# Performance work log

Measured on AMD Instinct MI355X. Metric: run time of the kernel, lower is better.

## Reference

```python
import jax, jax.numpy as jnp
import numpy as np

EPS = 1e-5

def bn(x, g, b, m, v):
    # inference-mode BatchNorm2d over channel dim
    return (x - m[None, :, None, None]) * jax.lax.rsqrt(v[None, :, None, None] + EPS) * g[None, :, None, None] + b[None, :, None, None]

def conv1x1(x, W, b=None):
    y = jnp.einsum('oc,bchw->bohw', W, x)
    return y + b[None, :, None, None] if b is not None else y

def forward(x, W3, b3, g1, b1, m1, v1, Wa, ba, g2, b2, m2, v2, Wq, bq, Wk, bk, Wv, bv, gam, Wg, bg, g3, b3n, m3, v3, Wf, bf, g4, b4, m4, v4, Wr, rs):
    B, C, H, Wd = x.shape
    N = H * Wd
    # conv branch: 3x3 conv + BN + ReLU
    y3 = jax.lax.conv_general_dilated(x, W3, (1, 1), ((1, 1), (1, 1)), dimension_numbers=('NCHW', 'OIHW', 'NCHW'))
    local = jax.nn.relu(bn(y3 + b3[None, :, None, None], g1, b1, m1, v1))
    # attn branch: 1x1 conv + BN + ReLU, then full-resolution attention
    a = jax.nn.relu(bn(conv1x1(x, Wa, ba), g2, b2, m2, v2))
    q = conv1x1(a, Wq, bq).reshape(B, -1, N)   # [B, C/8, N]
    k = conv1x1(a, Wk, bk).reshape(B, -1, N)   # [B, C/8, N]
    v = conv1x1(a, Wv, bv).reshape(B, -1, N)   # [B, C, N]
    att = jax.nn.softmax(jnp.einsum('bcn,bcm->bnm', q, k), axis=-1)  # [B, N, N], unscaled as in source
    o = jnp.einsum('bcm,bnm->bcn', v, att).reshape(a.shape)
    attn_feat = gam * o + a
    # gated fusion
    combined = jnp.concatenate([local, attn_feat], axis=1)
    gate = jax.nn.sigmoid(bn(conv1x1(combined, Wg, bg), g3, b3n, m3, v3))
    fused = gate * local + (1.0 - gate) * attn_feat
    out = jax.nn.relu(bn(conv1x1(jnp.concatenate([fused, combined], axis=1), Wf, bf), g4, b4, m4, v4))
    res = conv1x1(x, Wr)  # residual 1x1 conv, no bias (in != out channels)
    return out + rs * res

def setup_inputs() -> dict:
    B, Ci, Co, H, W_ = 4, 64, 128, 64, 64
    Cq = Co // 8
    ks = jax.random.split(jax.random.key(0), 24)
    def rn(i, s, sc=0.05):
        return jax.random.normal(ks[i], s, jnp.float32) * sc
    def var(i, c):
        return jax.random.uniform(ks[i], (c,), jnp.float32, 0.5, 1.5)
    ones = lambda c: jnp.ones((c,), jnp.float32)
    zeros = lambda c: jnp.zeros((c,), jnp.float32)
    return {
        'x': rn(0, (B, Ci, H, W_), 1.0),
        'W3': rn(1, (Co, Ci, 3, 3)), 'b3': rn(2, (Co,)),
        'g1': ones(Co), 'b1': zeros(Co), 'm1': rn(3, (Co,), 0.1), 'v1': var(4, Co),
        'Wa': rn(5, (Co, Ci)), 'ba': rn(6, (Co,)),
        'g2': ones(Co), 'b2': zeros(Co), 'm2': rn(7, (Co,), 0.1), 'v2': var(8, Co),
        'Wq': rn(9, (Cq, Co)), 'bq': rn(10, (Cq,)),
        'Wk': rn(11, (Cq, Co)), 'bk': rn(12, (Cq,)),
        'Wv': rn(13, (Co, Co)), 'bv': rn(14, (Co,)),
        'gam': jnp.array(0.5, jnp.float32),
        'Wg': rn(15, (Co, 2 * Co)), 'bg': rn(16, (Co,)),
        'g3': ones(Co), 'b3n': zeros(Co), 'm3': rn(17, (Co,), 0.1), 'v3': var(18, Co),
        'Wf': rn(19, (Co, 3 * Co)), 'bf': rn(20, (Co,)),
        'g4': ones(Co), 'b4': zeros(Co), 'm4': rn(21, (Co,), 0.1), 'v4': var(22, Co),
        'Wr': rn(23, (Co, Ci)),
        'rs': jnp.array(0.1, jnp.float32),
    }

def reference(x, W3, b3, g1, b1, m1, v1, Wa, ba, g2, b2, m2, v2, Wq, bq, Wk, bk, Wv, bv, gam, Wg, bg, g3, b3n, m3, v3, Wf, bf, g4, b4, m4, v4, Wr, rs):
    return forward(x, W3, b3, g1, b1, m1, v1, Wa, ba, g2, b2, m2, v2, Wq, bq, Wk, bk, Wv, bv, gam, Wg, bg, g3, b3n, m3, v3, Wf, bf, g4, b4, m4, v4, Wr, rs)
```

## Files before the change

### kernel.cpp

```cpp
#include <hip/hip_runtime.h>
#include <hip/hip_bf16.h>

#define CI_ 64
#define CO_ 128
#define NPIX 4096
#define CQ_ 16
#define EPS_ 1e-5f

typedef __attribute__((ext_vector_type(8))) __bf16 bf16x8;
typedef __attribute__((ext_vector_type(4))) __bf16 bf16x4;
typedef __attribute__((ext_vector_type(4))) float f32x4;

__global__ __launch_bounds__(256) void z_prepx(
    const float* __restrict__ x, __bf16* __restrict__ xT)
{
    __shared__ float tl[64][65];
    int b = blockIdx.x >> 6;
    int n0 = (blockIdx.x & 63) * 64;
    int tid = threadIdx.x;
    int nn = tid & 63, c4 = tid >> 6;
#pragma unroll
    for (int p = 0; p < 16; ++p) {
        int ci = p * 4 + c4;
        tl[ci][nn] = x[((size_t)b * CI_ + ci) * NPIX + n0 + nn];
    }
    __syncthreads();
#pragma unroll
    for (int p = 0; p < 2; ++p) {
        int idx = p * 256 + tid;
        int n = idx >> 3, cig = idx & 7;
        bf16x8 vv;
#pragma unroll
        for (int j = 0; j < 8; ++j) vv[j] = (__bf16)tl[cig * 8 + j][n];
        ((bf16x8*)xT)[((size_t)b * NPIX + n0 + n) * 8 + cig] = vv;
    }
}

__global__ __launch_bounds__(256) void z_prepw(
    const float* __restrict__ W3, __bf16* __restrict__ Wt2)
{
    int o = blockIdx.x * 256 + threadIdx.x;
    int co = o / 576;
    int r = o - co * 576;
    int tap = r >> 6;
    int ci = r & 63;
    Wt2[o] = (__bf16)W3[((size_t)co * CI_ + ci) * 9 + tap];
}

__global__ __launch_bounds__(256) void z_prepfw2(
    const float* __restrict__ Wg, const float* __restrict__ Wf, const float* __restrict__ Wr,
    const float* __restrict__ Wa, const float* __restrict__ Wq, const float* __restrict__ Wk,
    const float* __restrict__ Wv, __bf16* __restrict__ Wb)
{
    int i = blockIdx.x * 256 + threadIdx.x;
    if (i >= 118784) return;
    float val;
    if (i < 32768) val = Wg[i];
    else if (i < 81920) val = Wf[i - 32768];
    else if (i < 90112) val = Wr[i - 81920];
    else if (i < 98304) val = Wa[i - 90112];
    else if (i < 100352) val = Wq[i - 98304];
    else if (i < 102400) val = Wk[i - 100352];
    else val = Wv[i - 102400];
    Wb[i] = (__bf16)val;
}

__global__ __launch_bounds__(256) void z_mega(
    const __bf16* __restrict__ xT, const __bf16* __restrict__ Wb,
    const float* __restrict__ ba, const float* __restrict__ g2, const float* __restrict__ b2,
    const float* __restrict__ m2, const float* __restrict__ v2,
    const float* __restrict__ bq, const float* __restrict__ bk, const float* __restrict__ bv,
    float* __restrict__ a, float* __restrict__ q, __bf16* __restrict__ kT, __bf16* __restrict__ V2)
{
    __shared__ __align__(16) __bf16 an[16 * 128];
    int tid = threadIdx.x;
    int b = blockIdx.x >> 8;
    int n0 = (blockIdx.x & 255) * 16;
    int l = tid & 63, w = tid >> 6;
    int lm = l & 15, g = l >> 4;

    const __bf16* Wa2 = Wb + 90112;
    const __bf16* Wq2 = Wb + 98304;
    const __bf16* Wk2 = Wb + 100352;
    const __bf16* Wv2 = Wb + 102400;

    bf16x8 bx[2];
#pragma unroll
    for (int kc = 0; kc < 2; ++kc)
        bx[kc] = ((const bf16x8*)xT)[((size_t)b * NPIX + n0 + lm) * 8 + (kc * 4 + g)];
    f32x4 pa[2];
#pragma unroll
    for (int ct = 0; ct < 2; ++ct) {
#pragma unroll
        for (int r = 0; r < 4; ++r) pa[ct][r] = ba[w * 32 + ct * 16 + g * 4 + r];
#pragma unroll
        for (int kc = 0; kc < 2; ++kc) {
            bf16x8 afr = *(const bf16x8*)&Wa2[(size_t)(w * 32 + ct * 16 + lm) * 64 + kc * 32 + g * 8];
            pa[ct] = __builtin_amdgcn_mfma_f32_16x16x32_bf16(afr, bx[kc], pa[ct], 0, 0, 0);
        }
    }
#pragma unroll
    for (int ct = 0; ct < 2; ++ct) {
        bf16x4 pk;
#pragma unroll
        for (int r = 0; r < 4; ++r) {
            int co = w * 32 + ct * 16 + g * 4 + r;
            float sc = rsqrtf(v2[co] + EPS_) * g2[co];
            float sh = b2[co] - m2[co] * sc;
            float y = fmaxf(pa[ct][r] * sc + sh, 0.f);
            a[((size_t)b * CO_ + co) * NPIX + n0 + lm] = y;
            pk[r] = (__bf16)y;
        }
        int co8 = w * 4 + ct * 2 + (g >> 1);
        int ch = co8 ^ (lm & 7);
        *(bf16x4*)&an[lm * 128 + ch * 8 + (g & 1) * 4] = pk;
    }
    __syncthreads();

    bf16x8 bn[4];
#pragma unroll
    for (int kc = 0; kc < 4; ++kc) {
        int ch = (kc * 4 + g) ^ (lm & 7);
        bn[kc] = *(const bf16x8*)&an[lm * 128 + ch * 8];
    }
    f32x4 pv[2];
#pragma unroll
    for (int ct = 0; ct < 2; ++ct) {
#pragma unroll
        for (int r = 0; r < 4; ++r) pv[ct][r] = bv[w * 32 + ct * 16 + g * 4 + r];
#pragma unroll
        for (int kc = 0; kc < 4; ++kc) {
            bf16x8 afr = *(const bf16x8*)&Wv2[(size_t)(w * 32 + ct * 16 + lm) * 128 + kc * 32 + g * 8];
            pv[ct] = __builtin_amdgcn_mfma_f32_16x16x32_bf16(afr, bn[kc], pv[ct], 0, 0, 0);
        }
    }
    int n = n0 + lm;
#pragma unroll
    for (int ct = 0; ct < 2; ++ct)
#pragma unroll
        for (int r = 0; r < 4; ++r) {
            int c = w * 32 + ct * 16 + g * 4 + r;
            V2[(size_t)b * 524288 + (size_t)(n >> 3) * 1024 + c * 8 + (n & 7)] = (__bf16)pv[ct][r];
        }
    if (w == 0) {
        f32x4 pq;
#pragma unroll
        for (int r = 0; r < 4; ++r) pq[r] = bq[g * 4 + r];
#pragma unroll
        for (int kc = 0; kc < 4; ++kc) {
            bf16x8 afr = *(const bf16x8*)&Wq2[(size_t)lm * 128 + kc * 32 + g * 8];
            pq = __builtin_amdgcn_mfma_f32_16x16x32_bf16(afr, bn[kc], pq, 0, 0, 0);
        }
#pragma unroll
        for (int r = 0; r < 4; ++r)
            q[((size_t)b * CQ_ + g * 4 + r) * NPIX + n] = pq[r];
    } else if (w == 1) {
        f32x4 pk2;
#pragma unroll
        for (int r = 0; r < 4; ++r) pk2[r] = bk[g * 4 + r];
#pragma unroll
        for (int kc = 0; kc < 4; ++kc) {
            bf16x8 afr = *(const bf16x8*)&Wk2[(size_t)lm * 128 + kc * 32 + g * 8];
            pk2 = __builtin_amdgcn_mfma_f32_16x16x32_bf16(afr, bn[kc], pk2, 0, 0, 0);
        }
        bf16x4 kk;
#pragma unroll
        for (int r = 0; r < 4; ++r) kk[r] = (__bf16)pk2[r];
        *(bf16x4*)&kT[((size_t)b * NPIX + n) * CQ_ + g * 4] = kk;
    }
}

__global__ __launch_bounds__(256) void z_conv3m(
    const __bf16* __restrict__ xT, const __bf16* __restrict__ Wt2,
    const float* __restrict__ b3, const float* __restrict__ g,
    const float* __restrict__ bb, const float* __restrict__ m,
    const float* __restrict__ v, float* __restrict__ local)
{
    __shared__ __align__(16) __bf16 xt[3 * 66 * 64];
    __shared__ __align__(16) __bf16 wt[32 * 576];
    __shared__ float scs[32], shs[32];

    int blk = blockIdx.x;
    int b = blk >> 8;
    int h = (blk >> 2) & 63;
    int cg = blk & 3;
    int co0 = cg * 32;
    int tid = threadIdx.x;
    int l = tid & 63;
    int nt = tid >> 6;
    int lm = l & 15, lh = l >> 4;

    if (tid < 32) {
        int co = co0 + tid;
        float scv = rsqrtf(v[co] + EPS_) * g[co];
        scs[tid] = scv;
        shs[tid] = (b3[co] - m[co]) * scv + bb[co];
    }

    const bf16x8* xs = (const bf16x8*)xT + (size_t)b * (NPIX * 8);
    for (int i = tid; i < 1584; i += 256) {
        int r = i / 528;
        int rem = i - r * 528;
        int c = rem >> 3;
        int cig = rem & 7;
        int hh = h + r - 1;
        int gc = c - 1;
        bf16x8 val;
#pragma unroll
        for (int j = 0; j < 8; ++j) val[j] = (__bf16)0.f;
        if ((unsigned)hh < 64u && (unsigned)gc < 64u)
            val = xs[(hh * 64 + gc) * 8 + cig];
        *(bf16x8*)&xt[(r * 66 + c) * 64 + ((cig ^ (c & 7)) * 8)] = val;
    }
    const bf16x8* wsrc = (const bf16x8*)Wt2 + (size_t)co0 * 72;
    for (int i = tid; i < 2304; i += 256) {
        int co = i / 72;
        int kc = i - co * 72;
        *(bf16x8*)&wt[co * 576 + ((kc ^ (co & 7)) * 8)] = wsrc[i];
    }
    __syncthreads();

    f32x4 acc0 = {0.f, 0.f, 0.f, 0.f};
    f32x4 acc1 = {0.f, 0.f, 0.f, 0.f};
#pragma unroll
    for (int tap = 0; tap < 9; ++tap) {
        int dh = tap / 3, dw = tap % 3;
#pragma unroll
        for (int ks = 0; ks < 2; ++ks) {
            int cig = ks * 4 + lh;
            int col = nt * 16 + lm + dw;
            bf16x8 bfr = *(const bf16x8*)&xt[(dh * 66 + col) * 64 + ((cig ^ (col & 7)) * 8)];
            int kcg = tap * 8 + cig;
            bf16x8 a0 = *(const bf16x8*)&wt[lm * 576 + ((kcg ^ (lm & 7)) * 8)];
            bf16x8 a1 = *(const bf16x8*)&wt[(16 + lm) * 576 + ((kcg ^ (lm & 7)) * 8)];
            acc0 = __builtin_amdgcn_mfma_f32_16x16x32_bf16(a0, bfr, acc0, 0, 0, 0);
            acc1 = __builtin_amdgcn_mfma_f32_16x16x32_bf16(a1, bfr, acc1, 0, 0, 0);
        }
    }

    size_t obase = (size_t)b * CO_ * NPIX + h * 64 + nt * 16 + lm;
#pragma unroll
    for (int r = 0; r < 4; ++r) {
        int cl0 = lh * 4 + r;
        float y0 = fmaxf(acc0[r] * scs[cl0] + shs[cl0], 0.f);
        local[obase + (size_t)(co0 + cl0) * NPIX] = y0;
        int cl1 = 16 + cl0;
        float y1 = fmaxf(acc1[r] * scs[cl1] + shs[cl1], 0.f);
        local[obase + (size_t)(co0 + cl1) * NPIX] = y1;
    }
}

__global__ __launch_bounds__(256) void z_attn4s(
    const float* __restrict__ q, const __bf16* __restrict__ kT, const __bf16* __restrict__ V2,
    __bf16* __restrict__ o_part, float2* __restrict__ ml)
{
    __shared__ __align__(16) unsigned char smem[8704];
    __shared__ float wmax[4][16], wsum[4][16], fs[16];
    __bf16* p_lds = (__bf16*)smem;
    float* o_lds = (float*)smem;

    int tid = threadIdx.x;
    int b = blockIdx.x >> 9;
    int half = (blockIdx.x >> 8) & 1;
    int q0 = (blockIdx.x & 255) * 16;
    int l = tid & 63;
    int w = tid >> 6;
    int lm = l & 15;
    int g = l >> 4;

    bf16x8 qfrag;
#pragma unroll
    for (int j = 0; j < 8; ++j) qfrag[j] = (__bf16)0.f;
    if (g < 2) {
#pragma unroll
        for (int j = 0; j < 8; ++j)
            qfrag[j] = (__bf16)q[((size_t)b * CQ_ + g * 8 + j) * NPIX + q0 + lm];
    }

    float m_run = -1e30f, l_run = 0.f;
    f32x4 acc0 = {0.f, 0.f, 0.f, 0.f};
    f32x4 acc1 = {0.f, 0.f, 0.f, 0.f};
    int c0 = w * 32 + lm;
    int c1 = c0 + 16;
    const bf16x8* vbase = (const bf16x8*)V2 + (size_t)b * 65536;
    const __bf16* ktb = kT + (size_t)b * NPIX * CQ_;

    for (int t = 0; t < 8; ++t) {
        int m0 = half * 2048 + t * 256;
        f32x4 sfr[4];
#pragma unroll
        for (int ms = 0; ms < 4; ++ms) {
            bf16x8 kf;
#pragma unroll
            for (int j = 0; j < 8; ++j) kf[j] = (__bf16)0.f;
            if (g < 2)
                kf = *(const bf16x8*)&ktb[(size_t)(m0 + w * 64 + ms * 16 + lm) * CQ_ + g * 8];
            f32x4 zz = {0.f, 0.f, 0.f, 0.f};
            sfr[ms] = __builtin_amdgcn_mfma_f32_16x16x32_bf16(kf, qfrag, zz, 0, 0, 0);
        }
        float pmax = -1e30f;
#pragma unroll
        for (int ms = 0; ms < 4; ++ms)
#pragma unroll
            for (int r = 0; r < 4; ++r) pmax = fmaxf(pmax, sfr[ms][r]);
        pmax = fmaxf(pmax, __shfl_xor(pmax, 16));
        pmax = fmaxf(pmax, __shfl_xor(pmax, 32));
        if (g == 0) wmax[w][lm] = pmax;
        __syncthreads();
        float tmax = fmaxf(fmaxf(wmax[0][lm], wmax[1][lm]), fmaxf(wmax[2][lm], wmax[3][lm]));
        float nm = fmaxf(m_run, tmax);
        float f = __expf(m_run - nm);
        m_run = nm;
        if (w == 0 && g == 0) fs[lm] = f;
        float psum = 0.f;
#pragma unroll
        for (int ms = 0; ms < 4; ++ms) {
            float p0 = __expf(sfr[ms][0] - nm);
            float p1 = __expf(sfr[ms][1] - nm);
            float p2 = __expf(sfr[ms][2] - nm);
            float p3 = __expf(sfr[ms][3] - nm);
            psum += (p0 + p1) + (p2 + p3);
            bf16x4 pk;
            pk[0] = (__bf16)p0; pk[1] = (__bf16)p1; pk[2] = (__bf16)p2; pk[3] = (__bf16)p3;
            *(bf16x4*)&p_lds[lm * 264 + w * 64 + ms * 16 + g * 4] = pk;
        }
        psum += __shfl_xor(psum, 16);
        psum += __shfl_xor(psum, 32);
        if (g == 0) wsum[w][lm] = psum;
        __syncthreads();
        float tsum = (wsum[0][lm] + wsum[1][lm]) + (wsum[2][lm] + wsum[3][lm]);
        l_run = l_run * f + tsum;
        float f0 = fs[g * 4 + 0], f1 = fs[g * 4 + 1], f2 = fs[g * 4 + 2], f3 = fs[g * 4 + 3];
        acc0[0] *= f0; acc0[1] *= f1; acc0[2] *= f2; acc0[3] *= f3;
        acc1[0] *= f0; acc1[1] *= f1; acc1[2] *= f2; acc1[3] *= f3;
#pragma unroll
        for (int ks = 0; ks < 8; ++ks) {
            bf16x8 afrag = *(const bf16x8*)&p_lds[lm * 264 + ks * 32 + g * 8];
            int msv = (m0 >> 3) + ks * 4 + g;
            bf16x8 bf0 = vbase[msv * 128 + c0];
            bf16x8 bf1 = vbase[msv * 128 + c1];
            acc0 = __builtin_amdgcn_mfma_f32_16x16x32_bf16(afrag, bf0, acc0, 0, 0, 0);
            acc1 = __builtin_amdgcn_mfma_f32_16x16x32_bf16(afrag, bf1, acc1, 0, 0, 0);
        }
        __syncthreads();
    }

#pragma unroll
    for (int r = 0; r < 4; ++r) {
        int qrow = g * 4 + r;
        o_lds[c0 * 17 + qrow] = acc0[r];
        o_lds[c1 * 17 + qrow] = acc1[r];
    }
    if (w == 0 && g == 0)
        ml[(size_t)(half * 4 + b) * NPIX + q0 + lm] = make_float2(m_run, l_run);
    __syncthreads();
    int qi = tid & 15;
    float inv = 1.f / l_run;
#pragma unroll
    for (int j = 0; j < 8; ++j) {
        int cc = (tid >> 4) + 16 * j;
        size_t idx = ((size_t)(half * 4 + b) * CO_ + cc) * NPIX + q0 + qi;
        o_part[idx] = (__bf16)(o_lds[cc * 17 + qi] * inv);
    }
}

__global__ __launch_bounds__(256) void z_acomb(
    const __bf16* __restrict__ o_part, const float2* __restrict__ ml,
    const float* __restrict__ a, const float* __restrict__ gamp, float* __restrict__ attn)
{
    int i = blockIdx.x * 256 + threadIdx.x;
    int n4 = (i & 1023) * 4;
    int co = (i >> 10) & (CO_ - 1);
    int b = i >> 17;
    float gam = gamp[0];
    bf16x4 o1 = *(const bf16x4*)&o_part[((size_t)b * CO_ + co) * NPIX + n4];
    bf16x4 o2 = *(const bf16x4*)&o_part[((size_t)(4 + b) * CO_ + co) * NPIX + n4];
    float4 av = *(const float4*)(a + ((size_t)b * CO_ + co) * NPIX + n4);
    float r[4], ai[4] = {av.x, av.y, av.z, av.w};
#pragma unroll
    for (int e = 0; e < 4; ++e) {
        float2 m1 = ml[(size_t)b * NPIX + n4 + e];
        float2 m2 = ml[(size_t)(4 + b) * NPIX + n4 + e];
        float mm = fmaxf(m1.x, m2.x);
        float w1 = m1.y * __expf(m1.x - mm);
        float w2 = m2.y * __expf(m2.x - mm);
        float o = ((float)o1[e] * w1 + (float)o2[e] * w2) / (w1 + w2);
        r[e] = gam * o + ai[e];
    }
    float4 rv = {r[0], r[1], r[2], r[3]};
    *(float4*)(attn + ((size_t)b * CO_ + co) * NPIX + n4) = rv;
}

__global__ __launch_bounds__(256) void z_fuseout2(
    const float* __restrict__ local, const float* __restrict__ attn, const float* __restrict__ x,
    const __bf16* __restrict__ Wb,
    const float* __restrict__ bg, const float* __restrict__ g3, const float* __restrict__ b3n,
    const float* __restrict__ m3, const float* __restrict__ v3,
    const float* __restrict__ bfb, const float* __restrict__ g4, const float* __restrict__ b4,
    const float* __restrict__ m4, const float* __restrict__ v4,
    const float* __restrict__ rsp, float* __restrict__ out)
{
    __shared__ __align__(16) unsigned char smem[32768 + 4096];
    __bf16* sb2 = (__bf16*)smem;
    __bf16* sxT = (__bf16*)(smem + 28672);

    int tid = threadIdx.x;
    int b = blockIdx.x >> 7;
    int n0 = (blockIdx.x & 127) * 32;

#pragma unroll
    for (int p = 0; p < 4; ++p) {
        int idx = p * 256 + tid;
        int c = idx >> 3, j = idx & 7;
        float lv[4], av[4];
        *(float4*)lv = *(const float4*)(local + ((size_t)b * CO_ + c) * NPIX + n0 + j * 4);
        *(float4*)av = *(const float4*)(attn + ((size_t)b * CO_ + c) * NPIX + n0 + j * 4);
#pragma unroll
        for (int e = 0; e < 4; ++e) {
            int n = j * 4 + e;
            int k1 = 128 + c, k2 = 256 + c;
            sb2[n * 448 + (((k1 >> 3) ^ (n & 7)) << 3) + (k1 & 7)] = (__bf16)lv[e];
            sb2[n * 448 + (((k2 >> 3) ^ (n & 7)) << 3) + (k2 & 7)] = (__bf16)av[e];
        }
    }
#pragma unroll
    for (int p = 0; p < 2; ++p) {
        int idx = p * 256 + tid;
        int c = idx >> 3, j = idx & 7;
        float xv[4];
        *(float4*)xv = *(const float4*)(x + ((size_t)b * CI_ + c) * NPIX + n0 + j * 4);
#pragma unroll
        for (int e = 0; e < 4; ++e) {
            int n = j * 4 + e;
            sxT[n * 64 + (((c >> 3) ^ (n & 7)) << 3) + (c & 7)] = (__bf16)xv[e];
        }
    }
    __syncthreads();

    int l = tid & 63, w = tid >> 6;
    int lm = l & 15, g = l >> 4;
    int co0 = w * 32;
    int t7 = lm & 7;

    f32x4 p1[2][2];
#pragma unroll
    for (int cs = 0; cs < 2; ++cs) {
        float bv = bg[co0 + cs * 16 + lm];
#pragma unroll
        for (int ns = 0; ns < 2; ++ns) {
            p1[ns][cs][0] = bv; p1[ns][cs][1] = bv; p1[ns][cs][2] = bv; p1[ns][cs][3] = bv;
        }
    }
    const __bf16* Wg2 = Wb;
#pragma unroll
    for (int kc = 0; kc < 8; ++kc) {
        int ch = (16 + kc * 4 + g) ^ t7;
        bf16x8 a0 = *(const bf16x8*)&sb2[lm * 448 + ch * 8];
        bf16x8 a1 = *(const bf16x8*)&sb2[(16 + lm) * 448 + ch * 8];
        bf16x8 b0 = *(const bf16x8*)&Wg2[(size_t)(co0 + lm) * 256 + kc * 32 + g * 8];
        bf16x8 b1 = *(const bf16x8*)&Wg2[(size_t)(co0 + 16 + lm) * 256 + kc * 32 + g * 8];
        p1[0][0] = __builtin_amdgcn_mfma_f32_16x16x32_bf16(a0, b0, p1[0][0], 0, 0, 0);
        p1[0][1] = __builtin_amdgcn_mfma_f32_16x16x32_bf16(a0, b1, p1[0][1], 0, 0, 0);
        p1[1][0] = __builtin_amdgcn_mfma_f32_16x16x32_bf16(a1, b0, p1[1][0], 0, 0, 0);
        p1[1][1] = __builtin_amdgcn_mfma_f32_16x16x32_bf16(a1, b1, p1[1][1], 0, 0, 0);
    }
#pragma unroll
    for (int cs = 0; cs < 2; ++cs) {
        int co = co0 + cs * 16 + lm;
        float sc3 = rsqrtf(v3[co] + EPS_) * g3[co];
        float sh3 = b3n[co] - m3[co] * sc3;
        int kl = 128 + co, ka = 256 + co;
#pragma unroll
        for (int ns = 0; ns < 2; ++ns)
#pragma unroll
            for (int r = 0; r < 4; ++r) {
                int n = ns * 16 + g * 4 + r;
                float z = p1[ns][cs][r] * sc3 + sh3;
                float gate = 1.f / (1.f + __expf(-z));
                float lv = (float)sb2[n * 448 + (((kl >> 3) ^ (n & 7)) << 3) + (kl & 7)];
                float av = (float)sb2[n * 448 + (((ka >> 3) ^ (n & 7)) << 3) + (ka & 7)];
                float fu = gate * lv + (1.f - gate) * av;
                sb2[n * 448 + (((co >> 3) ^ (n & 7)) << 3) + (co & 7)] = (__bf16)fu;
            }
    }
    __syncthreads();

    f32x4 p2[2][2], pr[2][2];
#pragma unroll
    for (int cs = 0; cs < 2; ++cs) {
        float bv = bfb[co0 + cs * 16 + lm];
#pragma unroll
        for (int ns = 0; ns < 2; ++ns) {
            p2[ns][cs][0] = bv; p2[ns][cs][1] = bv; p2[ns][cs][2] = bv; p2[ns][cs][3] = bv;
            pr[ns][cs] = (f32x4){0.f, 0.f, 0.f, 0.f};
        }
    }
    const __bf16* Wf2 = Wb + 32768;
    const __bf16* Wr2 = Wb + 81920;
#pragma unroll
    for (int kc = 0; kc < 12; ++kc) {
        int ch = (kc * 4 + g) ^ t7;
        bf16x8 a0 = *(const bf16x8*)&sb2[lm * 448 + ch * 8];
        bf16x8 a1 = *(const bf16x8*)&sb2[(16 + lm) * 448 + ch * 8];
        bf16x8 b0 = *(const bf16x8*)&Wf2[(size_t)(co0 + lm) * 384 + kc * 32 + g * 8];
        bf16x8 b1 = *(const bf16x8*)&Wf2[(size_t)(co0 + 16 + lm) * 384 + kc * 32 + g * 8];
        p2[0][0] = __builtin_amdgcn_mfma_f32_16x16x32_bf16(a0, b0, p2[0][0], 0, 0, 0);
        p2[0][1] = __builtin_amdgcn_mfma_f32_16x16x32_bf16(a0, b1, p2[0][1], 0, 0, 0);
        p2[1][0] = __builtin_amdgcn_mfma_f32_16x16x32_bf16(a1, b0, p2[1][0], 0, 0, 0);
        p2[1][1] = __builtin_amdgcn_mfma_f32_16x16x32_bf16(a1, b1, p2[1][1], 0, 0, 0);
    }
#pragma unroll
    for (int kc = 0; kc < 2; ++kc) {
        int ch = (kc * 4 + g) ^ t7;
        bf16x8 a0 = *(const bf16x8*)&sxT[lm * 64 + ch * 8];
        bf16x8 a1 = *(const bf16x8*)&sxT[(16 + lm) * 64 + ch * 8];
        bf16x8 b0 = *(const bf16x8*)&Wr2[(size_t)(co0 + lm) * 64 + kc * 32 + g * 8];
        bf16x8 b1 = *(const bf16x8*)&Wr2[(size_t)(co0 + 16 + lm) * 64 + kc * 32 + g * 8];
        pr[0][0] = __builtin_amdgcn_mfma_f32_16x16x32_bf16(a0, b0, pr[0][0], 0, 0, 0);
        pr[0][1] = __builtin_amdgcn_mfma_f32_16x16x32_bf16(a0, b1, pr[0][1], 0, 0, 0);
        pr[1][0] = __builtin_amdgcn_mfma_f32_16x16x32_bf16(a1, b0, pr[1][0], 0, 0, 0);
        pr[1][1] = __builtin_amdgcn_mfma_f32_16x16x32_bf16(a1, b1, pr[1][1], 0, 0, 0);
    }
    __syncthreads();

    float* o_lds = (float*)smem;
    float rsv = rsp[0];
#pragma unroll
    for (int cs = 0; cs < 2; ++cs) {
        int co = co0 + cs * 16 + lm;
        float sc4 = rsqrtf(v4[co] + EPS_) * g4[co];
        float sh4 = b4[co] - m4[co] * sc4;
#pragma unroll
        for (int ns = 0; ns < 2; ++ns)
#pragma unroll
            for (int r = 0; r < 4; ++r) {
                int n = ns * 16 + g * 4 + r;
                float o = fmaxf(p2[ns][cs][r] * sc4 + sh4, 0.f) + rsv * pr[ns][cs][r];
                o_lds[co * 36 + n] = o;
            }
    }
    __syncthreads();
    {
        int c = tid >> 1, h = tid & 1;
#pragma unroll
        for (int j2 = 0; j2 < 4; ++j2) {
            float4 vv = *(float4*)&o_lds[c * 36 + h * 16 + j2 * 4];
            *(float4*)(out + ((size_t)b * CO_ + c) * NPIX + n0 + h * 16 + j2 * 4) = vv;
        }
    }
}

extern "C" void kernel_launch(void* const* d_in, const int* in_sizes, int n_in,
                              void* d_out, int out_size, void* d_ws, size_t ws_size,
                              hipStream_t stream) {
    const float* x   = (const float*)d_in[0];
    const float* W3  = (const float*)d_in[1];
    const float* b3  = (const float*)d_in[2];
    const float* g1  = (const float*)d_in[3];
    const float* b1  = (const float*)d_in[4];
    const float* m1  = (const float*)d_in[5];
    const float* v1  = (const float*)d_in[6];
    const float* Wa  = (const float*)d_in[7];
    const float* ba  = (const float*)d_in[8];
    const float* g2  = (const float*)d_in[9];
    const float* b2  = (const float*)d_in[10];
    const float* m2  = (const float*)d_in[11];
    const float* v2  = (const float*)d_in[12];
    const float* Wq  = (const float*)d_in[13];
    const float* bq  = (const float*)d_in[14];
    const float* Wk  = (const float*)d_in[15];
    const float* bk  = (const float*)d_in[16];
    const float* Wv  = (const float*)d_in[17];
    const float* bv  = (const float*)d_in[18];
    const float* gam = (const float*)d_in[19];
    const float* Wg  = (const float*)d_in[20];
    const float* bg  = (const float*)d_in[21];
    const float* g3  = (const float*)d_in[22];
    const float* b3n = (const float*)d_in[23];
    const float* m3  = (const float*)d_in[24];
    const float* v3  = (const float*)d_in[25];
    const float* Wf  = (const float*)d_in[26];
    const float* bfb = (const float*)d_in[27];
    const float* g4  = (const float*)d_in[28];
    const float* b4  = (const float*)d_in[29];
    const float* m4  = (const float*)d_in[30];
    const float* v4  = (const float*)d_in[31];
    const float* Wr  = (const float*)d_in[32];
    const float* rs  = (const float*)d_in[33];

    float* ws    = (float*)d_ws;
    float* a_    = ws;
    float* local = ws + 2097152;
    float* attn  = ws + 4194304;
    __bf16* V2   = (__bf16*)(ws + 6291456);
    float* q     = ws + 7340032;
    __bf16* kT   = (__bf16*)(ws + 7602176);
    __bf16* xT   = (__bf16*)(ws + 7864320);
    __bf16* Wt2  = (__bf16*)(ws + 8388608);
    __bf16* Wb   = (__bf16*)(ws + 8450048);
    __bf16* o_part = (__bf16*)(ws + 8509440);
    float2* ml   = (float2*)(ws + 10606592);

    float* out = (float*)d_out;

    z_prepx<<<256, 256, 0, stream>>>(x, xT);
    z_prepw<<<288, 256, 0, stream>>>(W3, Wt2);
    z_prepfw2<<<464, 256, 0, stream>>>(Wg, Wf, Wr, Wa, Wq, Wk, Wv, Wb);
    z_mega<<<1024, 256, 0, stream>>>(xT, Wb, ba, g2, b2, m2, v2, bq, bk, bv, a_, q, kT, V2);
    z_attn4s<<<2048, 256, 0, stream>>>(q, kT, V2, o_part, ml);
    z_acomb<<<2048, 256, 0, stream>>>(o_part, ml, a_, gam, attn);
    z_conv3m<<<1024, 256, 0, stream>>>(xT, Wt2, b3, g1, b1, m1, v1, local);
    z_fuseout2<<<512, 256, 0, stream>>>(local, attn, x, Wb, bg, g3, b3n, m3, v3,
                                        bfb, g4, b4, m4, v4, rs, out);
}
```

Before: 122.5 us.

## Process two query tiles per attention block to reuse V loads; merge weight prep

The attention kernel now handles 32 queries per block as two 16-query tiles that share each V fragment load, halving the global V traffic per query and the grid size. The two weight-prep kernels are merged into one launch to save launch overhead. In exchange it uses more registers and LDS, adds extra barriers per iteration, and has fewer blocks to fill the GPU.

Measured after the change: 112.8 us. -7.9%, faster.

```diff
diff --git a/kernel.cpp b/kernel.cpp
--- a/kernel.cpp
+++ b/kernel.cpp
@@ -36,33 +36,31 @@
     }
 }
 
-__global__ __launch_bounds__(256) void z_prepw(
-    const float* __restrict__ W3, __bf16* __restrict__ Wt2)
-{
-    int o = blockIdx.x * 256 + threadIdx.x;
-    int co = o / 576;
-    int r = o - co * 576;
-    int tap = r >> 6;
-    int ci = r & 63;
-    Wt2[o] = (__bf16)W3[((size_t)co * CI_ + ci) * 9 + tap];
-}
-
-__global__ __launch_bounds__(256) void z_prepfw2(
+__global__ __launch_bounds__(256) void z_prepw2(
+    const float* __restrict__ W3, __bf16* __restrict__ Wt2,
     const float* __restrict__ Wg, const float* __restrict__ Wf, const float* __restrict__ Wr,
     const float* __restrict__ Wa, const float* __restrict__ Wq, const float* __restrict__ Wk,
     const float* __restrict__ Wv, __bf16* __restrict__ Wb)
 {
     int i = blockIdx.x * 256 + threadIdx.x;
-    if (i >= 118784) return;
-    float val;
-    if (i < 32768) val = Wg[i];
-    else if (i < 81920) val = Wf[i - 32768];
-    else if (i < 90112) val = Wr[i - 81920];
-    else if (i < 98304) val = Wa[i - 90112];
-    else if (i < 100352) val = Wq[i - 98304];
-    else if (i < 102400) val = Wk[i - 100352];
-    else val = Wv[i - 102400];
-    Wb[i] = (__bf16)val;
+    if (i < 73728) {
+        int co = i / 576;
+        int r = i - co * 576;
+        int tap = r >> 6;
+        int ci = r & 63;
+        Wt2[i] = (__bf16)W3[((size_t)co * CI_ + ci) * 9 + tap];
+    }
+    if (i < 118784) {
+        float val;
+        if (i < 32768) val = Wg[i];
+        else if (i < 81920) val = Wf[i - 32768];
+        else if (i < 90112) val = Wr[i - 81920];
+        else if (i < 98304) val = Wa[i - 90112];
+        else if (i < 100352) val = Wq[i - 98304];
+        else if (i < 102400) val = Wk[i - 100352];
+        else val = Wv[i - 102400];
+        Wb[i] = (__bf16)val;
+    }
 }
 
 __global__ __launch_bounds__(256) void z_mega(
@@ -250,36 +248,40 @@
     }
 }
 
-__global__ __launch_bounds__(256) void z_attn4s(
+__global__ __launch_bounds__(256) void z_attn8(
     const float* __restrict__ q, const __bf16* __restrict__ kT, const __bf16* __restrict__ V2,
     __bf16* __restrict__ o_part, float2* __restrict__ ml)
 {
-    __shared__ __align__(16) unsigned char smem[8704];
-    __shared__ float wmax[4][16], wsum[4][16], fs[16];
-    __bf16* p_lds = (__bf16*)smem;
+    __shared__ __align__(16) unsigned char smem[16896];
+    __shared__ float wmaxA[4][16], wsumA[4][16], fsA[16];
+    __shared__ float wmaxB[4][16], wsumB[4][16], fsB[16];
+    __bf16* pA = (__bf16*)smem;
+    __bf16* pB = (__bf16*)(smem + 8448);
     float* o_lds = (float*)smem;
 
     int tid = threadIdx.x;
-    int b = blockIdx.x >> 9;
-    int half = (blockIdx.x >> 8) & 1;
-    int q0 = (blockIdx.x & 255) * 16;
+    int b = blockIdx.x >> 8;
+    int half = (blockIdx.x >> 7) & 1;
+    int q0 = (blockIdx.x & 127) * 32;
     int l = tid & 63;
     int w = tid >> 6;
     int lm = l & 15;
     int g = l >> 4;
 
-    bf16x8 qfrag;
-#pragma unroll
-    for (int j = 0; j < 8; ++j) qfrag[j] = (__bf16)0.f;
+    bf16x8 qfA, qfB;
+#pragma unroll
+    for (int j = 0; j < 8; ++j) { qfA[j] = (__bf16)0.f; qfB[j] = (__bf16)0.f; }
     if (g < 2) {
 #pragma unroll
-        for (int j = 0; j < 8; ++j)
-            qfrag[j] = (__bf16)q[((size_t)b * CQ_ + g * 8 + j) * NPIX + q0 + lm];
-    }
-
-    float m_run = -1e30f, l_run = 0.f;
-    f32x4 acc0 = {0.f, 0.f, 0.f, 0.f};
-    f32x4 acc1 = {0.f, 0.f, 0.f, 0.f};
+        for (int j = 0; j < 8; ++j) {
+            qfA[j] = (__bf16)q[((size_t)b * CQ_ + g * 8 + j) * NPIX + q0 + lm];
+            qfB[j] = (__bf16)q[((size_t)b * CQ_ + g * 8 + j) * NPIX + q0 + 16 + lm];
+        }
+    }
+
+    float mA = -1e30f, lA = 0.f, mB = -1e30f, lB = 0.f;
+    f32x4 aA0 = {0.f,0.f,0.f,0.f}, aA1 = {0.f,0.f,0.f,0.f};
+    f32x4 aB0 = {0.f,0.f,0.f,0.f}, aB1 = {0.f,0.f,0.f,0.f};
     int c0 = w * 32 + lm;
     int c1 = c0 + 16;
     const bf16x8* vbase = (const bf16x8*)V2 + (size_t)b * 65536;
@@ -287,80 +289,157 @@
 
     for (int t = 0; t < 8; ++t) {
         int m0 = half * 2048 + t * 256;
-        f32x4 sfr[4];
-#pragma unroll
-        for (int ms = 0; ms < 4; ++ms) {
-            bf16x8 kf;
-#pragma unroll
-            for (int j = 0; j < 8; ++j) kf[j] = (__bf16)0.f;
-            if (g < 2)
-                kf = *(const bf16x8*)&ktb[(size_t)(m0 + w * 64 + ms * 16 + lm) * CQ_ + g * 8];
-            f32x4 zz = {0.f, 0.f, 0.f, 0.f};
-            sfr[ms] = __builtin_amdgcn_mfma_f32_16x16x32_bf16(kf, qfrag, zz, 0, 0, 0);
-        }
-        float pmax = -1e30f;
-#pragma unroll
-        for (int ms = 0; ms < 4; ++ms)
-#pragma unroll
-            for (int r = 0; r < 4; ++r) pmax = fmaxf(pmax, sfr[ms][r]);
-        pmax = fmaxf(pmax, __shfl_xor(pmax, 16));
-        pmax = fmaxf(pmax, __shfl_xor(pmax, 32));
-        if (g == 0) wmax[w][lm] = pmax;
-        __syncthreads();
-        float tmax = fmaxf(fmaxf(wmax[0][lm], wmax[1][lm]), fmaxf(wmax[2][lm], wmax[3][lm]));
-        float nm = fmaxf(m_run, tmax);
-        float f = __expf(m_run - nm);
-        m_run = nm;
-        if (w == 0 && g == 0) fs[lm] = f;
-        float psum = 0.f;
-#pragma unroll
-        for (int ms = 0; ms < 4; ++ms) {
-            float p0 = __expf(sfr[ms][0] - nm);
-            float p1 = __expf(sfr[ms][1] - nm);
-            float p2 = __expf(sfr[ms][2] - nm);
-            float p3 = __expf(sfr[ms][3] - nm);
-            psum += (p0 + p1) + (p2 + p3);
-            bf16x4 pk;
-            pk[0] = (__bf16)p0; pk[1] = (__bf16)p1; pk[2] = (__bf16)p2; pk[3] = (__bf16)p3;
-            *(bf16x4*)&p_lds[lm * 264 + w * 64 + ms * 16 + g * 4] = pk;
-        }
-        psum += __shfl_xor(psum, 16);
-        psum += __shfl_xor(psum, 32);
-        if (g == 0) wsum[w][lm] = psum;
-        __syncthreads();
-        float tsum = (wsum[0][lm] + wsum[1][lm]) + (wsum[2][lm] + wsum[3][lm]);
-        l_run = l_run * f + tsum;
-        float f0 = fs[g * 4 + 0], f1 = fs[g * 4 + 1], f2 = fs[g * 4 + 2], f3 = fs[g * 4 + 3];
-        acc0[0] *= f0; acc0[1] *= f1; acc0[2] *= f2; acc0[3] *= f3;
-        acc1[0] *= f0; acc1[1] *= f1; acc1[2] *= f2; acc1[3] *= f3;
-#pragma unroll
-        for (int ks = 0; ks < 8; ++ks) {
-            bf16x8 afrag = *(const bf16x8*)&p_lds[lm * 264 + ks * 32 + g * 8];
-            int msv = (m0 >> 3) + ks * 4 + g;
-            bf16x8 bf0 = vbase[msv * 128 + c0];
-            bf16x8 bf1 = vbase[msv * 128 + c1];
-            acc0 = __builtin_amdgcn_mfma_f32_16x16x32_bf16(afrag, bf0, acc0, 0, 0, 0);
-            acc1 = __builtin_amdgcn_mfma_f32_16x16x32_bf16(afrag, bf1, acc1, 0, 0, 0);
-        }
-        __syncthreads();
-    }
-
+        {
+            f32x4 sfr[4];
+#pragma unroll
+            for (int ms = 0; ms < 4; ++ms) {
+                bf16x8 kf;
+#pragma unroll
+                for (int j = 0; j < 8; ++j) kf[j] = (__bf16)0.f;
+                if (g < 2)
+                    kf = *(const bf16x8*)&ktb[(size_t)(m0 + w * 64 + ms * 16 + lm) * CQ_ + g * 8];
+                f32x4 zz = {0.f, 0.f, 0.f, 0.f};
+                sfr[ms] = __builtin_amdgcn_mfma_f32_16x16x32_bf16(kf, qfA, zz, 0, 0, 0);
+            }
+            float pmax = -1e30f;
+#pragma unroll
+            for (int ms = 0; ms < 4; ++ms)
+#pragma unroll
+                for (int r = 0; r < 4; ++r) pmax = fmaxf(pmax, sfr[ms][r]);
+            pmax = fmaxf(pmax, __shfl_xor(pmax, 16));
+            pmax = fmaxf(pmax, __shfl_xor(pmax, 32));
+            if (g == 0) wmaxA[w][lm] = pmax;
+            __syncthreads();
+            float tmax = fmaxf(fmaxf(wmaxA[0][lm], wmaxA[1][lm]), fmaxf(wmaxA[2][lm], wmaxA[3][lm]));
+            float nm = fmaxf(mA, tmax);
+            float f = __expf(mA - nm);
+            mA = nm;
+            if (w == 0 && g == 0) fsA[lm] = f;
+            float psum = 0.f;
+#pragma unroll
+            for (int ms = 0; ms < 4; ++ms) {
+                float p0 = __expf(sfr[ms][0] - nm);
+                float p1 = __expf(sfr[ms][1] - nm);
+                float p2 = __expf(sfr[ms][2] - nm);
+                float p3 = __expf(sfr[ms][3] - nm);
+                psum += (p0 + p1) + (p2 + p3);
+                bf16x4 pk;
+                pk[0] = (__bf16)p0; pk[1] = (__bf16)p1; pk[2] = (__bf16)p2; pk[3] = (__bf16)p3;
+                *(bf16x4*)&pA[lm * 264 + w * 64 + ms * 16 + g * 4] = pk;
+            }
+            psum += __shfl_xor(psum, 16);
+            psum += __shfl_xor(psum, 32);
+            if (g == 0) wsumA[w][lm] = psum;
+            __syncthreads();
+            float tsum = (wsumA[0][lm] + wsumA[1][lm]) + (wsumA[2][lm] + wsumA[3][lm]);
+            lA = lA * f + tsum;
+        }
+        {
+            f32x4 sfr[4];
+#pragma unroll
+            for (int ms = 0; ms < 4; ++ms) {
+                bf16x8 kf;
+#pragma unroll
+                for (int j = 0; j < 8; ++j) kf[j] = (__bf16)0.f;
+                if (g < 2)
+                    kf = *(const bf16x8*)&ktb[(size_t)(m0 + w * 64 + ms * 16 + lm) * CQ_ + g * 8];
+                f32x4 zz = {0.f, 0.f, 0.f, 0.f};
+                sfr[ms] = __builtin_amdgcn_mfma_f32_16x16x32_bf16(kf, qfB, zz, 0, 0, 0);
+            }
+            float pmax = -1e30f;
+#pragma unroll
+            for (int ms = 0; ms < 4; ++ms)
+#pragma unroll
+                for (int r = 0; r < 4; ++r) pmax = fmaxf(pmax, sfr[ms][r]);
+            pmax = fmaxf(pmax, __shfl_xor(pmax, 16));
+            pmax = fmaxf(pmax, __shfl_xor(pmax, 32));
+            if (g == 0) wmaxB[w][lm] = pmax;
+            __syncthreads();
+            float tmax = fmaxf(fmaxf(wmaxB[0][lm], wmaxB[1][lm]), fmaxf(wmaxB[2][lm], wmaxB[3][lm]));
+            float nm = fmaxf(mB, tmax);
+            float f = __expf(mB - nm);
+            mB = nm;
+            if (w == 0 && g == 0) fsB[lm] = f;
+            float psum = 0.f;
+#pragma unroll
+            for (int ms = 0; ms < 4; ++ms) {
+                float p0 = __expf(sfr[ms][0] - nm);
+                float p1 = __expf(sfr[ms][1] - nm);
+                float p2 = __expf(sfr[ms][2] - nm);
+                float p3 = __expf(sfr[ms][3] - nm);
+                psum += (p0 + p1) + (p2 + p3);
+                bf16x4 pk;
+                pk[0] = (__bf16)p0; pk[1] = (__bf16)p1; pk[2] = (__bf16)p2; pk[3] = (__bf16)p3;
+                *(bf16x4*)&pB[lm * 264 + w * 64 + ms * 16 + g * 4] = pk;
+            }
+            psum += __shfl_xor(psum, 16);
+            psum += __shfl_xor(psum, 32);
+            if (g == 0) wsumB[w][lm] = psum;
+            __syncthreads();
+            float tsum = (wsumB[0][lm] + wsumB[1][lm]) + (wsumB[2][lm] + wsumB[3][lm]);
+            lB = lB * f + tsum;
+        }
+        {
+            float fA0 = fsA[g * 4 + 0], fA1 = fsA[g * 4 + 1], fA2 = fsA[g * 4 + 2], fA3 = fsA[g * 4 + 3];
+            float fB0 = fsB[g * 4 + 0], fB1 = fsB[g * 4 + 1], fB2 = fsB[g * 4 + 2], fB3 = fsB[g * 4 + 3];
+            aA0[0] *= fA0; aA0[1] *= fA1; aA0[2] *= fA2; aA0[3] *= fA3;
+            aA1[0] *= fA0; aA1[1] *= fA1; aA1[2] *= fA2; aA1[3] *= fA3;
+            aB0[0] *= fB0; aB0[1] *= fB1; aB0[2] *= fB2; aB0[3] *= fB3;
+            aB1[0] *= fB0; aB1[1] *= fB1; aB1[2] *= fB2; aB1[3] *= fB3;
+#pragma unroll
+            for (int ks = 0; ks < 8; ++ks) {
+                int msv = (m0 >> 3) + ks * 4 + g;
+                bf16x8 bf0 = vbase[msv * 128 + c0];
+                bf16x8 bf1 = vbase[msv * 128 + c1];
+                bf16x8 afA = *(const bf16x8*)&pA[lm * 264 + ks * 32 + g * 8];
+                bf16x8 afB = *(const bf16x8*)&pB[lm * 264 + ks * 32 + g * 8];
+                aA0 = __builtin_amdgcn_mfma_f32_16x16x32_bf16(afA, bf0, aA0, 0, 0, 0);
+                aA1 = __builtin_amdgcn_mfma_f32_16x16x32_bf16(afA, bf1, aA1, 0, 0, 0);
+                aB0 = __builtin_amdgcn_mfma_f32_16x16x32_bf16(afB, bf0, aB0, 0, 0, 0);
+                aB1 = __builtin_amdgcn_mfma_f32_16x16x32_bf16(afB, bf1, aB1, 0, 0, 0);
+            }
+        }
+    }
+
+    __syncthreads();
 #pragma unroll
     for (int r = 0; r < 4; ++r) {
         int qrow = g * 4 + r;
-        o_lds[c0 * 17 + qrow] = acc0[r];
-        o_lds[c1 * 17 + qrow] = acc1[r];
+        o_lds[c0 * 17 + qrow] = aA0[r];
+        o_lds[c1 * 17 + qrow] = aA1[r];
     }
     if (w == 0 && g == 0)
-        ml[(size_t)(half * 4 + b) * NPIX + q0 + lm] = make_float2(m_run, l_run);
-    __syncthreads();
-    int qi = tid & 15;
-    float inv = 1.f / l_run;
-#pragma unroll
-    for (int j = 0; j < 8; ++j) {
-        int cc = (tid >> 4) + 16 * j;
-        size_t idx = ((size_t)(half * 4 + b) * CO_ + cc) * NPIX + q0 + qi;
-        o_part[idx] = (__bf16)(o_lds[cc * 17 + qi] * inv);
+        ml[(size_t)(half * 4 + b) * NPIX + q0 + lm] = make_float2(mA, lA);
+    __syncthreads();
+    {
+        int qi = tid & 15;
+        float inv = 1.f / lA;
+#pragma unroll
+        for (int j = 0; j < 8; ++j) {
+            int cc = (tid >> 4) + 16 * j;
+            size_t idx = ((size_t)(half * 4 + b) * CO_ + cc) * NPIX + q0 + qi;
+            o_part[idx] = (__bf16)(o_lds[cc * 17 + qi] * inv);
+        }
+    }
+    __syncthreads();
+#pragma unroll
+    for (int r = 0; r < 4; ++r) {
+        int qrow = g * 4 + r;
+        o_lds[c0 * 17 + qrow] = aB0[r];
+        o_lds[c1 * 17 + qrow] = aB1[r];
+    }
+    if (w == 0 && g == 0)
+        ml[(size_t)(half * 4 + b) * NPIX + q0 + 16 + lm] = make_float2(mB, lB);
+    __syncthreads();
+    {
+        int qi = tid & 15;
+        float inv = 1.f / lB;
+#pragma unroll
+        for (int j = 0; j < 8; ++j) {
+            int cc = (tid >> 4) + 16 * j;
+            size_t idx = ((size_t)(half * 4 + b) * CO_ + cc) * NPIX + q0 + 16 + qi;
+            o_part[idx] = (__bf16)(o_lds[cc * 17 + qi] * inv);
+        }
     }
 }
 
@@ -604,10 +683,9 @@
     float* out = (float*)d_out;
 
     z_prepx<<<256, 256, 0, stream>>>(x, xT);
-    z_prepw<<<288, 256, 0, stream>>>(W3, Wt2);
-    z_prepfw2<<<464, 256, 0, stream>>>(Wg, Wf, Wr, Wa, Wq, Wk, Wv, Wb);
+    z_prepw2<<<464, 256, 0, stream>>>(W3, Wt2, Wg, Wf, Wr, Wa, Wq, Wk, Wv, Wb);
     z_mega<<<1024, 256, 0, stream>>>(xT, Wb, ba, g2, b2, m2, v2, bq, bk, bv, a_, q, kT, V2);
-    z_attn4s<<<2048, 256, 0, stream>>>(q, kT, V2, o_part, ml);
+    z_attn8<<<1024, 256, 0, stream>>>(q, kT, V2, o_part, ml);
     z_acomb<<<2048, 256, 0, stream>>>(o_part, ml, a_, gam, attn);
     z_conv3m<<<1024, 256, 0, stream>>>(xT, Wt2, b3, g1, b1, m1, v1, local);
     z_fuseout2<<<512, 256, 0, stream>>>(local, attn, x, Wb, bg, g3, b3n, m3, v3,
```
